# Kernel optimization log

Measured on AMD Instinct MI355X. Metric: run time of the kernel, lower is better.

Reference implementation:

```python
import jax, jax.numpy as jnp
import numpy as np

B, C, L, H = 4, 128, 4096, 4
GROUPS, EPS = 32, 1e-5


def group_norm(x, gamma, beta):
    # x: [B, C, L]; normalize per (batch, group) over (C//G, L)
    b, c, l = x.shape
    xg = x.reshape(b, GROUPS, c // GROUPS, l)
    mu = jnp.mean(xg, axis=(2, 3), keepdims=True)
    var = jnp.var(xg, axis=(2, 3), keepdims=True)
    xn = ((xg - mu) * jax.lax.rsqrt(var + EPS)).reshape(b, c, l)
    return xn * gamma[None, :, None] + beta[None, :, None]


def setup_inputs() -> dict:
    key = jax.random.key(0)
    k1, k2, k3 = jax.random.split(key, 3)
    return {
        "x": jax.random.normal(k1, (B, C, L), dtype=jnp.float32),
        "w_qkv": jax.random.normal(k2, (3 * C, C), dtype=jnp.float32) * 0.02,
        "w_proj": jax.random.normal(k3, (C, C), dtype=jnp.float32) * 0.02,
        "b_proj": jnp.zeros((C,), dtype=jnp.float32),
        "gn_gamma": jnp.ones((C,), dtype=jnp.float32),
        "gn_beta": jnp.zeros((C,), dtype=jnp.float32),
    }


def reference(x, w_qkv, w_proj, b_proj, gn_gamma, gn_beta):
    b, c, l = x.shape
    hd = c // H
    h = group_norm(x, gn_gamma, gn_beta)
    # 1x1 conv == channel matmul: [B, 3C, L]
    qkv = jnp.einsum('oc,bcl->bol', w_qkv, h)
    # torch reshape(B*H, 3C/H, L).chunk(3, dim=1): per-head contiguous slices
    qkv = qkv.reshape(b, H, 3 * hd, l)
    q, k, v = qkv[:, :, :hd], qkv[:, :, hd:2 * hd], qkv[:, :, 2 * hd:]
    scale = 1.0 / np.sqrt(np.sqrt(hd)).astype(np.float32)
    attn = jnp.einsum('bhct,bhcs->bhts', q * scale, k * scale)
    attn = jax.nn.softmax(attn, axis=-1)
    o = jnp.einsum('bhts,bhcs->bhct', attn, v).reshape(b, c, l)
    o = jnp.einsum('oc,bcl->bol', w_proj, o) + b_proj[None, :, None]
    return o + x
```

## Files before the change

### kernel.cpp

```cpp
#include <hip/hip_runtime.h>
#include <hip/hip_bf16.h>
#include <cstdint>
#include <cstddef>


#define B_ 4
#define C_ 128
#define L_ 4096
#define H_ 4
#define HD_ 32
#define NG_ 32
#define CPG_ 4
#define EPS_ 1e-5f
#define QKSCALE_ 0.5050097650430367f

typedef __attribute__((ext_vector_type(8))) short bf16x8;
typedef __attribute__((ext_vector_type(8))) unsigned short u16x8;
typedef __attribute__((ext_vector_type(4))) float f32x4;
typedef __attribute__((ext_vector_type(16))) float f32x16;
typedef __attribute__((ext_vector_type(2))) _Float16 f16x2;
typedef __attribute__((ext_vector_type(4))) _Float16 f16x4;
typedef __attribute__((ext_vector_type(8))) _Float16 f16x8;
typedef __attribute__((ext_vector_type(2))) unsigned int u32x2;
typedef __attribute__((ext_vector_type(4))) unsigned int u32x4;

#if __has_builtin(__builtin_amdgcn_exp2f)
#define EXP2F(x) __builtin_amdgcn_exp2f(x)
#else
#define EXP2F(x) exp2f(x)
#endif

__device__ __forceinline__ float bu2f(unsigned short u) {
  return __builtin_bit_cast(float, (unsigned int)(((unsigned int)u) << 16));
}
__device__ __forceinline__ unsigned short f2bu(float f) {
  unsigned int u = __builtin_bit_cast(unsigned int, f);
  unsigned int r = (u + 0x7fffu + ((u >> 16) & 1u)) >> 16;
  return (unsigned short)r;
}
__device__ __forceinline__ float4 u42f4(ushort4 u) {
  return make_float4(bu2f(u.x), bu2f(u.y), bu2f(u.z), bu2f(u.w));
}
__device__ __forceinline__ unsigned int pkbf(float a, float b) {
  return (unsigned int)f2bu(a) | ((unsigned int)f2bu(b) << 16);
}
__device__ __forceinline__ f16x2 pkhf2(float a, float b) {
#if __has_builtin(__builtin_amdgcn_cvt_pkrtz)
  return __builtin_bit_cast(f16x2, __builtin_amdgcn_cvt_pkrtz(a, b));
#else
  f16x2 r;
  r[0] = (_Float16)a;
  r[1] = (_Float16)b;
  return r;
#endif
}
__device__ __forceinline__ unsigned int pkhf(float a, float b) {
  return __builtin_bit_cast(unsigned int, pkhf2(a, b));
}

__device__ __forceinline__ void gload16(const void* g, void* l) {
  __builtin_amdgcn_global_load_lds(
      (const __attribute__((address_space(1))) unsigned int*)g,
      (__attribute__((address_space(3))) unsigned int*)l, 16, 0, 0);
}

__device__ __forceinline__ bool detect_fast(const ushort* x) {
  __shared__ int flag_s;
  int t = threadIdx.x;
  if (t < 64) {
    int e = (x[t] >> 7) & 0xFF;
    unsigned long long m = __ballot((e < 64) || (e > 192));
    if (t == 0) flag_s = (__popcll(m) > 4) ? 1 : 0;
  }
  __syncthreads();
  return flag_s != 0;
}

__device__ __forceinline__ float4 ldx4(const void* x, size_t idx, bool f32) {
  if (f32) return *((const float4*)x + (idx >> 2));
  ushort4 u = *((const ushort4*)x + (idx >> 2));
  return u42f4(u);
}

__global__ __launch_bounds__(256) void gn_stats(const void* __restrict__ x,
                                                const void* __restrict__ wq,
                                                const void* __restrict__ wp,
                                                const void* __restrict__ bp,
                                                ushort* __restrict__ wq_b,
                                                ushort* __restrict__ wp_b,
                                                float* __restrict__ bp_f,
                                                float2* __restrict__ gpart) {
  bool f32 = detect_fast((const ushort*)x);
  int blk = blockIdx.x;
  int t = threadIdx.x;

  if (blk >= 256) {
    int i0 = ((blk - 256) * 256 + t) * 8;
#pragma unroll
    for (int k = 0; k < 8; ++k) {
      int i = i0 + k;
      if (i >= 65664) break;
      if (i < 49152) {
        wq_b[i] = f32 ? f2bu(((const float*)wq)[i]) : ((const ushort*)wq)[i];
      } else if (i < 65536) {
        int off = i - 49152;
        wp_b[off] = f32 ? f2bu(((const float*)wp)[off]) : ((const ushort*)wp)[off];
      } else {
        int off = i - 65536;
        bp_f[off] = f32 ? ((const float*)bp)[off] : bu2f(((const ushort*)bp)[off]);
      }
    }
    return;
  }

  int b = blk >> 6, rem = blk & 63;
  int g = rem >> 1, half = rem & 1;
  size_t base = ((size_t)b * C_ + (size_t)g * CPG_) * L_ + (size_t)half * 2048;

  float s = 0.f, ss = 0.f;
#pragma unroll
  for (int cc = 0; cc < 4; ++cc) {
#pragma unroll
    for (int i = 0; i < 2; ++i) {
      size_t e = base + (size_t)cc * L_ + i * 1024 + t * 4;
      float4 f = ldx4(x, e, f32);
      s += f.x + f.y + f.z + f.w;
      ss += f.x * f.x + f.y * f.y + f.z * f.z + f.w * f.w;
    }
  }
#pragma unroll
  for (int m = 32; m >= 1; m >>= 1) {
    s += __shfl_xor(s, m, 64);
    ss += __shfl_xor(ss, m, 64);
  }
  __shared__ float red[4][2];
  int wv = t >> 6;
  if ((t & 63) == 0) { red[wv][0] = s; red[wv][1] = ss; }
  __syncthreads();
  if (t == 0) {
    float ts = red[0][0] + red[1][0] + red[2][0] + red[3][0];
    float tss = red[0][1] + red[1][1] + red[2][1] + red[3][1];
    gpart[(b * 32 + g) * 2 + half] = make_float2(ts, tss);
  }
}

__global__ __launch_bounds__(256) void qkv_kernel(const ushort* __restrict__ wq_b,
                                                  const void* __restrict__ x,
                                                  const float2* __restrict__ gpart,
                                                  const void* __restrict__ gm,
                                                  const void* __restrict__ bt,
                                                  ushort* __restrict__ Qt,
                                                  ushort* __restrict__ Kt,
                                                  ushort* __restrict__ Vb) {
  bool f32 = detect_fast((const ushort*)x);
  __shared__ alignas(16) ushort Hs[64][136];
  __shared__ alignas(16) float Ls[64][69];
  __shared__ float2 abs_s[128];

  int lx = blockIdx.x, oz = blockIdx.y, b = blockIdx.z;
  int t = threadIdx.x;
  int w = t >> 6, lane = t & 63, l16 = lane & 15, q = lane >> 4, q8 = q * 8;

  if (t < 64) {
#pragma unroll
    for (int k = 0; k < 2; ++k) {
      int c = 2 * t + k;
      int g = c >> 2;
      float2 p0 = gpart[(b * 32 + g) * 2];
      float2 p1 = gpart[(b * 32 + g) * 2 + 1];
      float mu = (p0.x + p1.x) * (1.0f / 16384.0f);
      float var = (p0.y + p1.y) * (1.0f / 16384.0f) - mu * mu;
      float rs = rsqrtf(var + EPS_);
      float ga = f32 ? ((const float*)gm)[c] : bu2f(((const ushort*)gm)[c]);
      float be = f32 ? ((const float*)bt)[c] : bu2f(((const ushort*)bt)[c]);
      abs_s[c] = make_float2(ga * rs, be - mu * ga * rs);
    }
  }
  __syncthreads();

  {
    int u = t & 63, lh = (t >> 6) * 16;
    int c0 = 2 * u;
    float2 ab0 = abs_s[c0];
    float2 ab1 = abs_s[c0 + 1];
    size_t xo = ((size_t)b * C_ + c0) * L_ + (size_t)lx * 64 + lh;
#pragma unroll
    for (int j = 0; j < 4; ++j) {
      float4 f0 = ldx4(x, xo + j * 4, f32);
      float4 f1 = ldx4(x, xo + L_ + j * 4, f32);
      float n0[4] = {f0.x * ab0.x + ab0.y, f0.y * ab0.x + ab0.y,
                     f0.z * ab0.x + ab0.y, f0.w * ab0.x + ab0.y};
      float n1[4] = {f1.x * ab1.x + ab1.y, f1.y * ab1.x + ab1.y,
                     f1.z * ab1.x + ab1.y, f1.w * ab1.x + ab1.y};
#pragma unroll
      for (int k = 0; k < 4; ++k)
        *(unsigned int*)&Hs[lh + j * 4 + k][c0] = pkbf(n0[k], n1[k]);
    }
  }
  __syncthreads();

  for (int j = 0; j < 2; ++j) {
    int oy = oz * 2 + j;
    const ushort* wg = wq_b + (size_t)(oy * 64 + w * 16 + l16) * C_;

    f32x4 acc[4] = {{0.f, 0.f, 0.f, 0.f}, {0.f, 0.f, 0.f, 0.f},
                    {0.f, 0.f, 0.f, 0.f}, {0.f, 0.f, 0.f, 0.f}};
#pragma unroll
    for (int kc = 0; kc < 4; ++kc) {
      bf16x8 aw = *(const bf16x8*)(wg + kc * 32 + q8);
#pragma unroll
      for (int nb = 0; nb < 4; ++nb) {
        bf16x8 bh = *(const bf16x8*)&Hs[nb * 16 + l16][kc * 32 + q8];
        acc[nb] = __builtin_amdgcn_mfma_f32_16x16x32_bf16(aw, bh, acc[nb], 0, 0, 0);
      }
    }
    __syncthreads();
#pragma unroll
    for (int nb = 0; nb < 4; ++nb)
#pragma unroll
      for (int r = 0; r < 4; ++r)
        Ls[nb * 16 + l16][w * 16 + 4 * q + r] = acc[nb][r];
    __syncthreads();

#pragma unroll
    for (int hhalf = 0; hhalf < 2; ++hhalf) {
      int hh = oy * 2 + hhalf;
      int type = hh % 3, head = hh / 3;
      size_t bh = (size_t)b * H_ + head;
      if (type == 2) {
        int c_loc = t >> 3, l8 = (t & 7) * 8;
        float v[8];
#pragma unroll
        for (int jj = 0; jj < 8; ++jj) v[jj] = Ls[l8 + jj][hhalf * 32 + c_loc];
        uint4 u;
        u.x = pkhf(v[0], v[1]);
        u.y = pkhf(v[2], v[3]);
        u.z = pkhf(v[4], v[5]);
        u.w = pkhf(v[6], v[7]);
        *(uint4*)(Vb + (bh * 32 + c_loc) * L_ + (size_t)lx * 64 + l8) = u;
      } else {
        ushort* dst = type ? Kt : Qt;
        int l = t >> 2, seg = (t & 3) * 8;
        const float* src = &Ls[l][hhalf * 32 + seg];
        uint4 u;
        u.x = pkbf(src[0] * QKSCALE_, src[1] * QKSCALE_);
        u.y = pkbf(src[2] * QKSCALE_, src[3] * QKSCALE_);
        u.z = pkbf(src[4] * QKSCALE_, src[5] * QKSCALE_);
        u.w = pkbf(src[6] * QKSCALE_, src[7] * QKSCALE_);
        *(uint4*)(dst + ((bh * L_) + lx * 64 + l) * 32 + seg) = u;
      }
    }
  }
}

__global__ __launch_bounds__(512) void attn_kernel(const ushort* __restrict__ Qt,
                                                   const ushort* __restrict__ Kt,
                                                   const ushort* __restrict__ Vb,
                                                   ushort* __restrict__ ot) {
  __shared__ alignas(16) char smem[65536];

  int t = threadIdx.x;
  int w = t >> 6, lane = t & 63, l31 = lane & 31, hi = lane >> 5;
  int qt = w & 3, sh = w >> 2;
  int tq0 = blockIdx.x * 128;
  int bh = blockIdx.y;
  int b = bh >> 2, head = bh & 3;
  const ushort* Qg = Qt + ((size_t)bh * L_ + tq0) * 32;
  const ushort* Kg = Kt + (size_t)bh * L_ * 32;
  const ushort* Vg = Vb + (size_t)bh * 32 * L_;

  int rd = t >> 2, pd = t & 3;
  int kcsem = (pd - rd) & 3;
  const ushort* ksrc = Kg + (size_t)rd * 32 + kcsem * 8;
  int vr = t >> 4, vp = t & 15;
  int vcsem = (vp & 8) | ((vp & 7) ^ (vr & 7));
  const ushort* vsrc = Vg + (size_t)vr * L_ + vcsem * 8;

  const ushort* qbase = Qg + (size_t)(qt * 32 + l31) * 32;
  bf16x8 qB0 = *(const bf16x8*)(qbase + 8 * hi);
  bf16x8 qB1 = *(const bf16x8*)(qbase + 16 + 8 * hi);

  const f16x2 one2 = {(_Float16)1.0f, (_Float16)1.0f};

#pragma unroll
  for (int s = 0; s < 3; ++s) {
    gload16(ksrc, smem + s * 8192 + (size_t)t * 16);
    gload16(vsrc, smem + 32768 + s * 8192 + (size_t)t * 16);
    ksrc += 4096;
    vsrc += 128;
  }

  f32x16 aO = {0.f};
  float lsum = 0.f;

  for (int it = 0; it < 32; ++it) {
    int rem = 31 - it;
    if (rem >= 2) {
      asm volatile("s_waitcnt vmcnt(4)" ::: "memory");
    } else if (rem == 1) {
      asm volatile("s_waitcnt vmcnt(2)" ::: "memory");
    } else {
      asm volatile("s_waitcnt vmcnt(0)" ::: "memory");
    }
    __builtin_amdgcn_sched_barrier(0);
    __builtin_amdgcn_s_barrier();
    __builtin_amdgcn_sched_barrier(0);

    if (it < 29) {
      char* kd = smem + ((it + 3) & 3) * 8192;
      char* vd = smem + 32768 + ((it + 3) & 3) * 8192;
      gload16(ksrc, kd + (size_t)t * 16);
      gload16(vsrc, vd + (size_t)t * 16);
      ksrc += 4096;
      vsrc += 128;
    }

    const ushort* kc = (const ushort*)(smem + (it & 3) * 8192);
    const ushort* vc = (const ushort*)(smem + 32768 + (it & 3) * 8192);

#pragma unroll
    for (int st = 0; st < 2; ++st) {
      int s0 = 64 * sh + 32 * st;
      const ushort* krow = kc + (size_t)(s0 + l31) * 32;
      bf16x8 aK0 = *(const bf16x8*)(krow + ((hi + l31) & 3) * 8);
      bf16x8 aK1 = *(const bf16x8*)(krow + ((2 + hi + l31) & 3) * 8);
      f32x16 zz = {0.f};
      f32x16 sf;
      __builtin_amdgcn_s_setprio(1);
      sf = __builtin_amdgcn_mfma_f32_32x32x16_bf16(aK0, qB0, zz, 0, 0, 0);
      sf = __builtin_amdgcn_mfma_f32_32x32x16_bf16(aK1, qB1, sf, 0, 0, 0);
      __builtin_amdgcn_s_setprio(0);

#pragma unroll
      for (int sb = 0; sb < 2; ++sb) {
        int sblk = 4 * sh + 2 * st + sb;
        int kci = 2 * sblk + hi;
        int vpos = (kci & 8) | ((kci & 7) ^ (l31 & 7));
        f16x8 vf = *(const f16x8*)(vc + (size_t)l31 * 128 + vpos * 8);

        float p0 = EXP2F(sf[8 * sb + 0]);
        float p1 = EXP2F(sf[8 * sb + 1]);
        float p2 = EXP2F(sf[8 * sb + 2]);
        float p3 = EXP2F(sf[8 * sb + 3]);
        float p4 = EXP2F(sf[8 * sb + 4]);
        float p5 = EXP2F(sf[8 * sb + 5]);
        float p6 = EXP2F(sf[8 * sb + 6]);
        float p7 = EXP2F(sf[8 * sb + 7]);
        f16x2 cA0 = pkhf2(p0, p1), cA1 = pkhf2(p2, p3);
        f16x2 cB0 = pkhf2(p4, p5), cB1 = pkhf2(p6, p7);
        lsum = __builtin_amdgcn_fdot2(cA0, one2, lsum, false);
        lsum = __builtin_amdgcn_fdot2(cA1, one2, lsum, false);
        lsum = __builtin_amdgcn_fdot2(cB0, one2, lsum, false);
        lsum = __builtin_amdgcn_fdot2(cB1, one2, lsum, false);

        u32x2 r0 = __builtin_amdgcn_permlane32_swap(
            __builtin_bit_cast(unsigned int, cA0),
            __builtin_bit_cast(unsigned int, cB0), false, false);
        u32x2 r1 = __builtin_amdgcn_permlane32_swap(
            __builtin_bit_cast(unsigned int, cA1),
            __builtin_bit_cast(unsigned int, cB1), false, false);
        u32x4 pw = {r0.x, r1.x, r0.y, r1.y};
        f16x8 pf = __builtin_bit_cast(f16x8, pw);

        __builtin_amdgcn_s_setprio(1);
        aO = __builtin_amdgcn_mfma_f32_32x32x16_f16(vf, pf, aO, 0, 0, 0);
        __builtin_amdgcn_s_setprio(0);
      }
    }
  }
  __syncthreads();

  float* Osh = (float*)smem;
  float* Lp = (float*)(smem + 33792);
  {
    float* ob = Osh + (size_t)(sh * 4 + qt) * (32 * 33) + (size_t)l31 * 33;
#pragma unroll
    for (int reg = 0; reg < 16; ++reg) {
      int R = (reg & 3) + 8 * (reg >> 2) + 4 * hi;
      ob[R] = aO[reg];
    }
    Lp[(sh * 2 + hi) * 128 + qt * 32 + l31] = lsum;
  }
  __syncthreads();

  {
    int qloc = t >> 2, c0 = (t & 3) * 8;
    int qt2 = qloc >> 5, q31 = qloc & 31;
    float lt = Lp[qloc] + Lp[128 + qloc] + Lp[256 + qloc] + Lp[384 + qloc];
    float inv = 1.0f / lt;
    const float* o0 = Osh + (size_t)qt2 * (32 * 33) + (size_t)q31 * 33 + c0;
    const float* o1 = o0 + 4 * (32 * 33);
    float o[8];
#pragma unroll
    for (int jj = 0; jj < 8; ++jj) o[jj] = (o0[jj] + o1[jj]) * inv;
    uint4 u;
    u.x = pkbf(o[0], o[1]);
    u.y = pkbf(o[2], o[3]);
    u.z = pkbf(o[4], o[5]);
    u.w = pkbf(o[6], o[7]);
    *(uint4*)(ot + ((size_t)b * L_ + tq0 + qloc) * C_ + head * 32 + c0) = u;
  }
}

__global__ __launch_bounds__(256) void proj_kernel(const ushort* __restrict__ wp_b,
                                                   const float* __restrict__ bias,
                                                   const void* __restrict__ x,
                                                   const ushort* __restrict__ ot,
                                                   void* __restrict__ out) {
  bool f32 = detect_fast((const ushort*)x);
  __shared__ alignas(16) float Ls[64][37];

  int lx = blockIdx.x, oy = blockIdx.y, b = blockIdx.z;
  int t = threadIdx.x;
  int w = t >> 6, lane = t & 63, l16 = lane & 15, q = lane >> 4, q8 = q * 8;

  const ushort* wg = wp_b + (size_t)(oy * 64 + w * 16 + l16) * C_;
  const ushort* og = ot + ((size_t)b * L_ + (size_t)lx * 32) * C_;

  f32x4 acc[2] = {{0.f, 0.f, 0.f, 0.f}, {0.f, 0.f, 0.f, 0.f}};
#pragma unroll
  for (int kc = 0; kc < 4; ++kc) {
    bf16x8 aw = *(const bf16x8*)(wg + kc * 32 + q8);
#pragma unroll
    for (int nb = 0; nb < 2; ++nb) {
      bf16x8 bo = *(const bf16x8*)(og + (size_t)(nb * 16 + l16) * C_ + kc * 32 + q8);
      acc[nb] = __builtin_amdgcn_mfma_f32_16x16x32_bf16(aw, bo, acc[nb], 0, 0, 0);
    }
  }
#pragma unroll
  for (int nb = 0; nb < 2; ++nb)
#pragma unroll
    for (int r = 0; r < 4; ++r)
      Ls[w * 16 + 4 * q + r][nb * 16 + l16] = acc[nb][r];
  __syncthreads();

  {
    int o_loc = t >> 2, ls0 = (t & 3) * 8;
    float bv = bias[oy * 64 + o_loc];
    size_t off = ((size_t)b * C_ + oy * 64 + o_loc) * L_ + (size_t)lx * 32 + ls0;
#pragma unroll
    for (int jj = 0; jj < 2; ++jj) {
      float4 xf = ldx4(x, off + jj * 4, f32);
      const float* sp = &Ls[o_loc][ls0 + jj * 4];
      float4 r = make_float4(sp[0] + bv + xf.x, sp[1] + bv + xf.y,
                             sp[2] + bv + xf.z, sp[3] + bv + xf.w);
      if (f32) {
        *(float4*)((float*)out + off + jj * 4) = r;
      } else {
        *(ushort4*)((ushort*)out + off + jj * 4) =
            make_ushort4(f2bu(r.x), f2bu(r.y), f2bu(r.z), f2bu(r.w));
      }
    }
  }
}

extern "C" void kernel_launch(void* const* d_in, const int* in_sizes, int n_in,
                              void* d_out, int out_size, void* d_ws, size_t ws_size,
                              hipStream_t stream) {
  const void* x      = d_in[0];
  const void* w_qkv  = d_in[1];
  const void* w_proj = d_in[2];
  const void* b_proj = d_in[3];
  const void* gamma  = d_in[4];
  const void* beta   = d_in[5];

  char* wsb = (char*)d_ws;
  ushort* wq_b  = (ushort*)(wsb + 0);
  ushort* wp_b  = (ushort*)(wsb + 98304);
  float*  bp_f  = (float*)(wsb + 131072);
  float2* gpart = (float2*)(wsb + 131584);
  ushort* Qt    = (ushort*)(wsb + 8388608);
  ushort* Kt    = (ushort*)(wsb + 12582912);
  ushort* Vb    = (ushort*)(wsb + 16777216);
  ushort* ot    = (ushort*)(wsb + 20971520);

  gn_stats<<<dim3(289), dim3(256), 0, stream>>>(x, w_qkv, w_proj, b_proj,
                                                wq_b, wp_b, bp_f, gpart);
  qkv_kernel<<<dim3(L_ / 64, 3, B_), dim3(256), 0, stream>>>(wq_b, x, gpart, gamma, beta,
                                                             Qt, Kt, Vb);
  attn_kernel<<<dim3(L_ / 128, B_ * H_), dim3(512), 0, stream>>>(Qt, Kt, Vb, ot);
  proj_kernel<<<dim3(L_ / 32, C_ / 64, B_), dim3(256), 0, stream>>>(wp_b, bp_f, x, ot, d_out);
}
```

Baseline: 140.5 us.

## Shrink attention query tile to 64 and double-buffer K/V for occupancy

The attention kernel now handles 64 queries per block instead of 128, with 8 waves split as 2 query tiles by 4 key slices. Shared memory drops from 64KB to 35KB with two K/V buffers instead of four, and launch bounds request more resident blocks. This doubles the grid size so more blocks fit per CU. In exchange, each K/V tile fetched from memory is reused by fewer queries, prefetch depth falls to one stage, and a full __syncthreads now runs on every iteration.

```diff
diff --git a/kernel.cpp b/kernel.cpp
--- a/kernel.cpp
+++ b/kernel.cpp
@@ -253,16 +253,16 @@
   }
 }
 
-__global__ __launch_bounds__(512) void attn_kernel(const ushort* __restrict__ Qt,
-                                                   const ushort* __restrict__ Kt,
-                                                   const ushort* __restrict__ Vb,
-                                                   ushort* __restrict__ ot) {
-  __shared__ alignas(16) char smem[65536];
+__global__ __launch_bounds__(512, 8) void attn_kernel(const ushort* __restrict__ Qt,
+                                                      const ushort* __restrict__ Kt,
+                                                      const ushort* __restrict__ Vb,
+                                                      ushort* __restrict__ ot) {
+  __shared__ alignas(16) char smem[35840];
 
   int t = threadIdx.x;
   int w = t >> 6, lane = t & 63, l31 = lane & 31, hi = lane >> 5;
-  int qt = w & 3, sh = w >> 2;
-  int tq0 = blockIdx.x * 128;
+  int qt = w & 1, sh = w >> 1;
+  int tq0 = blockIdx.x * 64;
   int bh = blockIdx.y;
   int b = bh >> 2, head = bh & 3;
   const ushort* Qg = Qt + ((size_t)bh * L_ + tq0) * 32;
@@ -270,135 +270,125 @@
   const ushort* Vg = Vb + (size_t)bh * 32 * L_;
 
   int rd = t >> 2, pd = t & 3;
-  int kcsem = (pd - rd) & 3;
+  int kcsem = (pd - (rd >> 1)) & 3;
   const ushort* ksrc = Kg + (size_t)rd * 32 + kcsem * 8;
   int vr = t >> 4, vp = t & 15;
   int vcsem = (vp & 8) | ((vp & 7) ^ (vr & 7));
   const ushort* vsrc = Vg + (size_t)vr * L_ + vcsem * 8;
 
+  char* kb0 = smem;
+  char* kb1 = smem + 8192;
+  char* vb0 = smem + 16384;
+  char* vb1 = smem + 24576;
+
   const ushort* qbase = Qg + (size_t)(qt * 32 + l31) * 32;
   bf16x8 qB0 = *(const bf16x8*)(qbase + 8 * hi);
   bf16x8 qB1 = *(const bf16x8*)(qbase + 16 + 8 * hi);
 
   const f16x2 one2 = {(_Float16)1.0f, (_Float16)1.0f};
-
-#pragma unroll
-  for (int s = 0; s < 3; ++s) {
-    gload16(ksrc, smem + s * 8192 + (size_t)t * 16);
-    gload16(vsrc, smem + 32768 + s * 8192 + (size_t)t * 16);
-    ksrc += 4096;
-    vsrc += 128;
-  }
+  const f32x16 zz = {0.f};
+
+  gload16(ksrc, kb0 + (size_t)t * 16);
+  gload16(vsrc, vb0 + (size_t)t * 16);
+  ksrc += 4096;
+  vsrc += 128;
+  __syncthreads();
 
   f32x16 aO = {0.f};
   float lsum = 0.f;
-
+  int s0 = 32 * sh;
+  int rot = (l31 >> 1) & 3;
+
+  int flip = 0;
   for (int it = 0; it < 32; ++it) {
-    int rem = 31 - it;
-    if (rem >= 2) {
-      asm volatile("s_waitcnt vmcnt(4)" ::: "memory");
-    } else if (rem == 1) {
-      asm volatile("s_waitcnt vmcnt(2)" ::: "memory");
-    } else {
-      asm volatile("s_waitcnt vmcnt(0)" ::: "memory");
-    }
-    __builtin_amdgcn_sched_barrier(0);
-    __builtin_amdgcn_s_barrier();
-    __builtin_amdgcn_sched_barrier(0);
-
-    if (it < 29) {
-      char* kd = smem + ((it + 3) & 3) * 8192;
-      char* vd = smem + 32768 + ((it + 3) & 3) * 8192;
-      gload16(ksrc, kd + (size_t)t * 16);
-      gload16(vsrc, vd + (size_t)t * 16);
+    if (it < 31) {
+      gload16(ksrc, (flip ? kb0 : kb1) + (size_t)t * 16);
+      gload16(vsrc, (flip ? vb0 : vb1) + (size_t)t * 16);
       ksrc += 4096;
       vsrc += 128;
     }
-
-    const ushort* kc = (const ushort*)(smem + (it & 3) * 8192);
-    const ushort* vc = (const ushort*)(smem + 32768 + (it & 3) * 8192);
-
-#pragma unroll
-    for (int st = 0; st < 2; ++st) {
-      int s0 = 64 * sh + 32 * st;
-      const ushort* krow = kc + (size_t)(s0 + l31) * 32;
-      bf16x8 aK0 = *(const bf16x8*)(krow + ((hi + l31) & 3) * 8);
-      bf16x8 aK1 = *(const bf16x8*)(krow + ((2 + hi + l31) & 3) * 8);
-      f32x16 zz = {0.f};
-      f32x16 sf;
+    const ushort* kc = (const ushort*)(flip ? kb1 : kb0);
+    const ushort* vc = (const ushort*)(flip ? vb1 : vb0);
+
+    const ushort* krow = kc + (size_t)(s0 + l31) * 32;
+    bf16x8 aK0 = *(const bf16x8*)(krow + ((hi + rot) & 3) * 8);
+    bf16x8 aK1 = *(const bf16x8*)(krow + ((2 + hi + rot) & 3) * 8);
+    f32x16 sf;
+    __builtin_amdgcn_s_setprio(1);
+    sf = __builtin_amdgcn_mfma_f32_32x32x16_bf16(aK0, qB0, zz, 0, 0, 0);
+    sf = __builtin_amdgcn_mfma_f32_32x32x16_bf16(aK1, qB1, sf, 0, 0, 0);
+    __builtin_amdgcn_s_setprio(0);
+
+#pragma unroll
+    for (int sb = 0; sb < 2; ++sb) {
+      int sblk = 2 * sh + sb;
+      int kci = 2 * sblk + hi;
+      int vpos = (kci & 8) | ((kci & 7) ^ (l31 & 7));
+      f16x8 vf = *(const f16x8*)(vc + (size_t)l31 * 128 + vpos * 8);
+
+      float p0 = EXP2F(sf[8 * sb + 0]);
+      float p1 = EXP2F(sf[8 * sb + 1]);
+      float p2 = EXP2F(sf[8 * sb + 2]);
+      float p3 = EXP2F(sf[8 * sb + 3]);
+      float p4 = EXP2F(sf[8 * sb + 4]);
+      float p5 = EXP2F(sf[8 * sb + 5]);
+      float p6 = EXP2F(sf[8 * sb + 6]);
+      float p7 = EXP2F(sf[8 * sb + 7]);
+      f16x2 cA0 = pkhf2(p0, p1), cA1 = pkhf2(p2, p3);
+      f16x2 cB0 = pkhf2(p4, p5), cB1 = pkhf2(p6, p7);
+      lsum = __builtin_amdgcn_fdot2(cA0, one2, lsum, false);
+      lsum = __builtin_amdgcn_fdot2(cA1, one2, lsum, false);
+      lsum = __builtin_amdgcn_fdot2(cB0, one2, lsum, false);
+      lsum = __builtin_amdgcn_fdot2(cB1, one2, lsum, false);
+
+      u32x2 r0 = __builtin_amdgcn_permlane32_swap(
+          __builtin_bit_cast(unsigned int, cA0),
+          __builtin_bit_cast(unsigned int, cB0), false, false);
+      u32x2 r1 = __builtin_amdgcn_permlane32_swap(
+          __builtin_bit_cast(unsigned int, cA1),
+          __builtin_bit_cast(unsigned int, cB1), false, false);
+      u32x4 pw = {r0.x, r1.x, r0.y, r1.y};
+      f16x8 pf = __builtin_bit_cast(f16x8, pw);
+
       __builtin_amdgcn_s_setprio(1);
-      sf = __builtin_amdgcn_mfma_f32_32x32x16_bf16(aK0, qB0, zz, 0, 0, 0);
-      sf = __builtin_amdgcn_mfma_f32_32x32x16_bf16(aK1, qB1, sf, 0, 0, 0);
+      aO = __builtin_amdgcn_mfma_f32_32x32x16_f16(vf, pf, aO, 0, 0, 0);
       __builtin_amdgcn_s_setprio(0);
-
-#pragma unroll
-      for (int sb = 0; sb < 2; ++sb) {
-        int sblk = 4 * sh + 2 * st + sb;
-        int kci = 2 * sblk + hi;
-        int vpos = (kci & 8) | ((kci & 7) ^ (l31 & 7));
-        f16x8 vf = *(const f16x8*)(vc + (size_t)l31 * 128 + vpos * 8);
-
-        float p0 = EXP2F(sf[8 * sb + 0]);
-        float p1 = EXP2F(sf[8 * sb + 1]);
-        float p2 = EXP2F(sf[8 * sb + 2]);
-        float p3 = EXP2F(sf[8 * sb + 3]);
-        float p4 = EXP2F(sf[8 * sb + 4]);
-        float p5 = EXP2F(sf[8 * sb + 5]);
-        float p6 = EXP2F(sf[8 * sb + 6]);
-        float p7 = EXP2F(sf[8 * sb + 7]);
-        f16x2 cA0 = pkhf2(p0, p1), cA1 = pkhf2(p2, p3);
-        f16x2 cB0 = pkhf2(p4, p5), cB1 = pkhf2(p6, p7);
-        lsum = __builtin_amdgcn_fdot2(cA0, one2, lsum, false);
-        lsum = __builtin_amdgcn_fdot2(cA1, one2, lsum, false);
-        lsum = __builtin_amdgcn_fdot2(cB0, one2, lsum, false);
-        lsum = __builtin_amdgcn_fdot2(cB1, one2, lsum, false);
-
-        u32x2 r0 = __builtin_amdgcn_permlane32_swap(
-            __builtin_bit_cast(unsigned int, cA0),
-            __builtin_bit_cast(unsigned int, cB0), false, false);
-        u32x2 r1 = __builtin_amdgcn_permlane32_swap(
-            __builtin_bit_cast(unsigned int, cA1),
-            __builtin_bit_cast(unsigned int, cB1), false, false);
-        u32x4 pw = {r0.x, r1.x, r0.y, r1.y};
-        f16x8 pf = __builtin_bit_cast(f16x8, pw);
-
-        __builtin_amdgcn_s_setprio(1);
-        aO = __builtin_amdgcn_mfma_f32_32x32x16_f16(vf, pf, aO, 0, 0, 0);
-        __builtin_amdgcn_s_setprio(0);
-      }
-    }
-  }
-  __syncthreads();
+    }
+    __syncthreads();
+    flip ^= 1;
+  }
 
   float* Osh = (float*)smem;
   float* Lp = (float*)(smem + 33792);
   {
-    float* ob = Osh + (size_t)(sh * 4 + qt) * (32 * 33) + (size_t)l31 * 33;
+    float* ob = Osh + (size_t)(sh * 2 + qt) * (32 * 33) + (size_t)l31 * 33;
 #pragma unroll
     for (int reg = 0; reg < 16; ++reg) {
       int R = (reg & 3) + 8 * (reg >> 2) + 4 * hi;
       ob[R] = aO[reg];
     }
-    Lp[(sh * 2 + hi) * 128 + qt * 32 + l31] = lsum;
+    Lp[(sh * 2 + hi) * 64 + qt * 32 + l31] = lsum;
   }
   __syncthreads();
 
   {
-    int qloc = t >> 2, c0 = (t & 3) * 8;
+    int qloc = t >> 3, seg = (t & 7) * 4;
     int qt2 = qloc >> 5, q31 = qloc & 31;
-    float lt = Lp[qloc] + Lp[128 + qloc] + Lp[256 + qloc] + Lp[384 + qloc];
+    float lt = 0.f;
+#pragma unroll
+    for (int k = 0; k < 8; ++k) lt += Lp[k * 64 + qloc];
     float inv = 1.0f / lt;
-    const float* o0 = Osh + (size_t)qt2 * (32 * 33) + (size_t)q31 * 33 + c0;
-    const float* o1 = o0 + 4 * (32 * 33);
-    float o[8];
-#pragma unroll
-    for (int jj = 0; jj < 8; ++jj) o[jj] = (o0[jj] + o1[jj]) * inv;
-    uint4 u;
-    u.x = pkbf(o[0], o[1]);
-    u.y = pkbf(o[2], o[3]);
-    u.z = pkbf(o[4], o[5]);
-    u.w = pkbf(o[6], o[7]);
-    *(uint4*)(ot + ((size_t)b * L_ + tq0 + qloc) * C_ + head * 32 + c0) = u;
+    float o[4] = {0.f, 0.f, 0.f, 0.f};
+#pragma unroll
+    for (int s = 0; s < 4; ++s) {
+      const float* op = Osh + (size_t)(s * 2 + qt2) * (32 * 33) + (size_t)q31 * 33 + seg;
+#pragma unroll
+      for (int jj = 0; jj < 4; ++jj) o[jj] += op[jj];
+    }
+    uint2 u;
+    u.x = pkbf(o[0] * inv, o[1] * inv);
+    u.y = pkbf(o[2] * inv, o[3] * inv);
+    *(uint2*)(ot + ((size_t)b * L_ + tq0 + qloc) * C_ + head * 32 + seg) = u;
   }
 }
 
@@ -478,6 +468,6 @@
                                                 wq_b, wp_b, bp_f, gpart);
   qkv_kernel<<<dim3(L_ / 64, 3, B_), dim3(256), 0, stream>>>(wq_b, x, gpart, gamma, beta,
                                                              Qt, Kt, Vb);
-  attn_kernel<<<dim3(L_ / 128, B_ * H_), dim3(512), 0, stream>>>(Qt, Kt, Vb, ot);
+  attn_kernel<<<dim3(L_ / 64, B_ * H_), dim3(512), 0, stream>>>(Qt, Kt, Vb, ot);
   proj_kernel<<<dim3(L_ / 32, C_ / 64, B_), dim3(256), 0, stream>>>(wp_b, bp_f, x, ot, d_out);
 }
```

Measured after the change: 141.6 us. Within noise of the previous version (+0.8%).
